# Kernel optimization log

Measured on AMD Instinct MI355X. Metric: run time of the kernel, lower is better.

Reference implementation:

```python
import jax, jax.numpy as jnp
import numpy as np

N_RAY, N_SAMPLES = 131072, 128
BIG_DELTA = 1e10
EPS = 1e-10


def setup_inputs() -> dict:
    key = jax.random.key(0)
    k1, k2, k3 = jax.random.split(key, 3)
    rgb = jax.random.uniform(k1, (N_RAY, N_SAMPLES, 3), dtype=jnp.float32)
    sigma = jax.random.normal(k2, (N_RAY, N_SAMPLES), dtype=jnp.float32)
    # sorted depths per ray in [2.0, 6.0), mimicking near/far bounds
    z_raw = jax.random.uniform(k3, (N_RAY, N_SAMPLES), dtype=jnp.float32, minval=2.0, maxval=6.0)
    z_vals = jnp.sort(z_raw, axis=-1)
    return {"rgb": rgb, "sigma": sigma, "z_vals": z_vals, "white_bkgd": 1}


def reference(rgb, sigma, z_vals, white_bkgd):
    # deltas: distance between adjacent samples, last one set to a huge value
    deltas = z_vals[:, 1:] - z_vals[:, :-1]
    deltas = jnp.concatenate(
        [deltas, jnp.full_like(deltas[:, :1], BIG_DELTA)], axis=-1)
    # sigma_activation = relu (opt.sigma_activation == 'relu')
    alpha = 1.0 - jnp.exp(-deltas * jax.nn.relu(sigma))
    # exclusive cumulative product of transmittance
    accum_prod = jnp.concatenate(
        [jnp.ones_like(alpha[:, :1]),
         jnp.cumprod(1.0 - alpha[:, :-1] + EPS, axis=-1)], axis=-1)
    weights = alpha * accum_prod                    # [N_ray, N_samples]
    comp_rgb = jnp.einsum('ns,nsc->nc', weights, rgb)  # [N_ray, 3]
    depth = jnp.sum(weights * z_vals, axis=-1)         # [N_ray]
    opacity = jnp.sum(weights, axis=-1)                # [N_ray]
    if white_bkgd:
        comp_rgb = comp_rgb + (1.0 - opacity[:, None])
    return comp_rgb, depth, opacity, weights
```

## Files before the change

### kernel.cpp

```cpp
#include <hip/hip_runtime.h>

#define N_RAY 131072
#define NS 128
#define BIG_DELTA 1e10f
#define EPS 1e-10f

#define DPPF(OLD, V, CTRL, RM) \
  __int_as_float(__builtin_amdgcn_update_dpp(__float_as_int(OLD), __float_as_int(V), (CTRL), (RM), 0xf, false))

__device__ __forceinline__ float mul_scan_incl(float p) {
    p *= DPPF(1.0f, p, 0x111, 0xf);
    p *= DPPF(1.0f, p, 0x112, 0xf);
    p *= DPPF(1.0f, p, 0x114, 0xf);
    p *= DPPF(1.0f, p, 0x118, 0xf);
    p *= DPPF(1.0f, p, 0x142, 0xa);
    p *= DPPF(1.0f, p, 0x143, 0xc);
    return p;
}

__device__ __forceinline__ float wave_sum63(float v) {
    v += DPPF(0.0f, v, 0x111, 0xf);
    v += DPPF(0.0f, v, 0x112, 0xf);
    v += DPPF(0.0f, v, 0x114, 0xf);
    v += DPPF(0.0f, v, 0x118, 0xf);
    v += DPPF(0.0f, v, 0x142, 0xa);
    v += DPPF(0.0f, v, 0x143, 0xc);
    return v;
}

__global__ __launch_bounds__(256) void volrender_kernel(
    const float* __restrict__ rgb,
    const float* __restrict__ sigma,
    const float* __restrict__ z_vals,
    const int* __restrict__ wb_flag,
    float* __restrict__ out)
{
    const int tid  = blockIdx.x * blockDim.x + threadIdx.x;
    const int ray  = tid >> 6;
    const int lane = tid & 63;

    const size_t base = (size_t)ray * NS + 2 * lane;

    const float2 z  = *reinterpret_cast<const float2*>(&z_vals[base]);
    const float2 sg = *reinterpret_cast<const float2*>(&sigma[base]);
    const float* rp = rgb + (size_t)ray * (NS * 3) + 6 * lane;
    const float2 c01 = *reinterpret_cast<const float2*>(rp);
    const float2 c23 = *reinterpret_cast<const float2*>(rp + 2);
    const float2 c45 = *reinterpret_cast<const float2*>(rp + 4);

    float znext = DPPF(0.0f, z.x, 0x130, 0xf);
    float d0 = z.y - z.x;
    float d1 = (lane == 63) ? BIG_DELTA : (znext - z.y);

    float e0 = __expf(-d0 * fmaxf(sg.x, 0.0f));
    float e1 = __expf(-d1 * fmaxf(sg.y, 0.0f));
    float a0 = 1.0f - e0, a1 = 1.0f - e1;
    float t0 = e0 + EPS,  t1 = e1 + EPS;

    float p = mul_scan_incl(t0 * t1);
    float E = DPPF(1.0f, p, 0x138, 0xf);

    float w0 = a0 * E;
    float w1 = a1 * (E * t0);

    float* wout = out + (size_t)N_RAY * 5;
    *reinterpret_cast<float2*>(&wout[base]) = make_float2(w0, w1);

    float r   = w0 * c01.x + w1 * c23.y;
    float g   = w0 * c01.y + w1 * c45.x;
    float b   = w0 * c23.x + w1 * c45.y;
    float dep = w0 * z.x   + w1 * z.y;

    r   = wave_sum63(r);
    g   = wave_sum63(g);
    b   = wave_sum63(b);
    dep = wave_sum63(dep);

    if (lane == 63) {
        float op = 1.0f - p;
        const float add = (*wb_flag) ? (1.0f - op) : 0.0f;
        out[(size_t)ray * 3 + 0] = r + add;
        out[(size_t)ray * 3 + 1] = g + add;
        out[(size_t)ray * 3 + 2] = b + add;
        out[(size_t)N_RAY * 3 + ray] = dep;
        out[(size_t)N_RAY * 4 + ray] = op;
    }
}

extern "C" void kernel_launch(void* const* d_in, const int* in_sizes, int n_in,
                              void* d_out, int out_size, void* d_ws, size_t ws_size,
                              hipStream_t stream) {
    const float* rgb    = (const float*)d_in[0];
    const float* sigma  = (const float*)d_in[1];
    const float* z_vals = (const float*)d_in[2];
    const int*   wb     = (const int*)d_in[3];
    float* out = (float*)d_out;

    const int blocks = N_RAY / 4;
    volrender_kernel<<<blocks, 256, 0, stream>>>(rgb, sigma, z_vals, wb, out);
}
```

Baseline: 75.32 us.

## Use persistent waves with software-pipelined prefetch of next ray

Replaces the one-wave-per-ray launch with a fixed set of 8192 waves. Each wave loops over 16 rays and prefetches the next ray's z, sigma and rgb while computing the current one. The weights output is now written with nontemporal stores, and the white-background flag is read once per thread. The aim is to hide memory latency and cut launch and wave-scheduling overhead on a bandwidth-bound kernel, at the cost of fewer resident waves and higher register use.

```diff
diff --git a/kernel.cpp b/kernel.cpp
--- a/kernel.cpp
+++ b/kernel.cpp
@@ -4,6 +4,10 @@
 #define NS 128
 #define BIG_DELTA 1e10f
 #define EPS 1e-10f
+#define NWAVE 8192
+#define ITERS (N_RAY / NWAVE)
+
+typedef float f32x2 __attribute__((ext_vector_type(2)));
 
 #define DPPF(OLD, V, CTRL, RM) \
   __int_as_float(__builtin_amdgcn_update_dpp(__float_as_int(OLD), __float_as_int(V), (CTRL), (RM), 0xf, false))
@@ -28,6 +32,10 @@
     return v;
 }
 
+__device__ __forceinline__ float2 ld2(const float* p) {
+    return *reinterpret_cast<const float2*>(p);
+}
+
 __global__ __launch_bounds__(256) void volrender_kernel(
     const float* __restrict__ rgb,
     const float* __restrict__ sigma,
@@ -35,55 +43,74 @@
     const int* __restrict__ wb_flag,
     float* __restrict__ out)
 {
-    const int tid  = blockIdx.x * blockDim.x + threadIdx.x;
-    const int ray  = tid >> 6;
-    const int lane = tid & 63;
+    const int lane = threadIdx.x & 63;
+    const int wid  = (blockIdx.x * blockDim.x + threadIdx.x) >> 6;
+    const int wb   = *wb_flag;
+    float* wout = out + (size_t)N_RAY * 5;
 
-    const size_t base = (size_t)ray * NS + 2 * lane;
+    size_t ray = wid;
 
-    const float2 z  = *reinterpret_cast<const float2*>(&z_vals[base]);
-    const float2 sg = *reinterpret_cast<const float2*>(&sigma[base]);
-    const float* rp = rgb + (size_t)ray * (NS * 3) + 6 * lane;
-    const float2 c01 = *reinterpret_cast<const float2*>(rp);
-    const float2 c23 = *reinterpret_cast<const float2*>(rp + 2);
-    const float2 c45 = *reinterpret_cast<const float2*>(rp + 4);
+    float2 z  = ld2(&z_vals[ray * NS + 2 * lane]);
+    float2 sg = ld2(&sigma [ray * NS + 2 * lane]);
+    const float* rp = rgb + ray * (NS * 3) + 6 * lane;
+    float2 c01 = ld2(rp), c23 = ld2(rp + 2), c45 = ld2(rp + 4);
 
-    float znext = DPPF(0.0f, z.x, 0x130, 0xf);
-    float d0 = z.y - z.x;
-    float d1 = (lane == 63) ? BIG_DELTA : (znext - z.y);
+    #pragma unroll 2
+    for (int it = 0; it < ITERS; ++it) {
+        float2 zn, sn, n01, n23, n45;
+        const size_t nray = ray + NWAVE;
+        if (it < ITERS - 1) {
+            zn = ld2(&z_vals[nray * NS + 2 * lane]);
+            sn = ld2(&sigma [nray * NS + 2 * lane]);
+            const float* np = rgb + nray * (NS * 3) + 6 * lane;
+            n01 = ld2(np); n23 = ld2(np + 2); n45 = ld2(np + 4);
+        }
 
-    float e0 = __expf(-d0 * fmaxf(sg.x, 0.0f));
-    float e1 = __expf(-d1 * fmaxf(sg.y, 0.0f));
-    float a0 = 1.0f - e0, a1 = 1.0f - e1;
-    float t0 = e0 + EPS,  t1 = e1 + EPS;
+        float znext = DPPF(0.0f, z.x, 0x130, 0xf);
+        float d0 = z.y - z.x;
+        float d1 = (lane == 63) ? BIG_DELTA : (znext - z.y);
 
-    float p = mul_scan_incl(t0 * t1);
-    float E = DPPF(1.0f, p, 0x138, 0xf);
+        float e0 = __expf(-d0 * fmaxf(sg.x, 0.0f));
+        float e1 = __expf(-d1 * fmaxf(sg.y, 0.0f));
+        float a0 = 1.0f - e0, a1 = 1.0f - e1;
+        float t0 = e0 + EPS,  t1 = e1 + EPS;
 
-    float w0 = a0 * E;
-    float w1 = a1 * (E * t0);
+        float p = mul_scan_incl(t0 * t1);
+        float E = DPPF(1.0f, p, 0x138, 0xf);
 
-    float* wout = out + (size_t)N_RAY * 5;
-    *reinterpret_cast<float2*>(&wout[base]) = make_float2(w0, w1);
+        float w0 = a0 * E;
+        float w1 = a1 * (E * t0);
 
-    float r   = w0 * c01.x + w1 * c23.y;
-    float g   = w0 * c01.y + w1 * c45.x;
-    float b   = w0 * c23.x + w1 * c45.y;
-    float dep = w0 * z.x   + w1 * z.y;
+        {
+            f32x2 wv; wv.x = w0; wv.y = w1;
+            __builtin_nontemporal_store(
+                wv, reinterpret_cast<f32x2*>(&wout[ray * NS + 2 * lane]));
+        }
 
-    r   = wave_sum63(r);
-    g   = wave_sum63(g);
-    b   = wave_sum63(b);
-    dep = wave_sum63(dep);
+        float r   = w0 * c01.x + w1 * c23.y;
+        float g   = w0 * c01.y + w1 * c45.x;
+        float b   = w0 * c23.x + w1 * c45.y;
+        float dep = w0 * z.x   + w1 * z.y;
 
-    if (lane == 63) {
-        float op = 1.0f - p;
-        const float add = (*wb_flag) ? (1.0f - op) : 0.0f;
-        out[(size_t)ray * 3 + 0] = r + add;
-        out[(size_t)ray * 3 + 1] = g + add;
-        out[(size_t)ray * 3 + 2] = b + add;
-        out[(size_t)N_RAY * 3 + ray] = dep;
-        out[(size_t)N_RAY * 4 + ray] = op;
+        r   = wave_sum63(r);
+        g   = wave_sum63(g);
+        b   = wave_sum63(b);
+        dep = wave_sum63(dep);
+
+        if (lane == 63) {
+            float op = 1.0f - p;
+            const float add = wb ? (1.0f - op) : 0.0f;
+            out[ray * 3 + 0] = r + add;
+            out[ray * 3 + 1] = g + add;
+            out[ray * 3 + 2] = b + add;
+            out[(size_t)N_RAY * 3 + ray] = dep;
+            out[(size_t)N_RAY * 4 + ray] = op;
+        }
+
+        if (it < ITERS - 1) {
+            z = zn; sg = sn; c01 = n01; c23 = n23; c45 = n45;
+        }
+        ray = nray;
     }
 }
 
@@ -96,6 +123,6 @@
     const int*   wb     = (const int*)d_in[3];
     float* out = (float*)d_out;
 
-    const int blocks = N_RAY / 4;
+    const int blocks = NWAVE / 4;
     volrender_kernel<<<blocks, 256, 0, stream>>>(rgb, sigma, z_vals, wb, out);
 }
```

After: 80.22 us. 1.07x slower.
